# Optimization experiments

Measured on AMD Instinct MI355X. Metric: run time of the kernel, lower is better.

## Reference

```python
import jax, jax.numpy as jnp
import numpy as np

B, T, E, H = 4, 1024, 512, 8
DH = E // H  # head dim = 64


def setup_inputs() -> dict:
    key = jax.random.key(0)
    ks = jax.random.split(key, 6)
    s = 1.0 / np.sqrt(E)
    return {
        "q": jax.random.normal(ks[0], (B, T, E), dtype=jnp.float32),
        "kv": jax.random.normal(ks[1], (B, T, E), dtype=jnp.float32),
        "Wq": jax.random.normal(ks[2], (E, E), dtype=jnp.float32) * s,
        "Wk": jax.random.normal(ks[3], (E, E), dtype=jnp.float32) * s,
        "Wv": jax.random.normal(ks[4], (E, E), dtype=jnp.float32) * s,
        "Wo": jax.random.normal(ks[5], (E, E), dtype=jnp.float32) * s,
        "head_num": H,
    }


def _split_heads_dh(x, h):
    # einops 'b t (d h)' with h=head_num: head index is FASTEST in channel dim
    b, t, e = x.shape
    d = e // h
    return x.reshape(b, t, d, h).transpose(0, 3, 1, 2)  # (b, h, t, d)


def reference(q, kv, Wq, Wk, Wv, Wo, head_num):
    e = q.shape[-1]
    dk = (e // head_num) ** 0.5  # NOTE: multiplied, per original code

    qp = q @ Wq   # weights stored as (in, out); Linear(bias=False)
    kp = kv @ Wk
    vp = kv @ Wv

    query = _split_heads_dh(qp, head_num)  # (b, h, t, d)
    key = _split_heads_dh(kp, head_num)
    value = _split_heads_dh(vp, head_num)

    qf = jnp.fft.fftn(query, axes=(-2, -1))  # complex, over (t, d)
    kf = jnp.fft.fftn(key, axes=(-2, -1))

    # complex einsum, key NOT conjugated (faithful to torch source)
    energy = jnp.einsum("bhid,bhjd->bhij", qf, kf) * dk
    energy = jnp.fft.ifftn(energy, axes=(-2, -1)).real  # (b, h, t, t)

    attention = jax.nn.softmax(energy, axis=-1)
    out = jnp.einsum("bhij,bhjd->bhid", attention, value)  # (b, h, t, d)

    # einops 'b h t d -> b t (h d)': head index SLOWEST in output channel dim
    b, h, t, d = out.shape
    out = out.transpose(0, 2, 1, 3).reshape(b, t, h * d)
    return out @ Wo
```

## Files before the change

### kernel.cpp

```cpp
#include <hip/hip_runtime.h>
#include <math.h>

#define BB 4
#define TT 1024
#define EE 512
#define HH 8
#define DD 64
#define BT (BB * TT)

typedef _Float16 f16;
typedef __attribute__((ext_vector_type(8))) _Float16 f16x8;
typedef __attribute__((ext_vector_type(4))) float f32x4;

__global__ __launch_bounds__(256) void prep_w_k(const float* __restrict__ Wq,
    const float* __restrict__ Wk, const float* __restrict__ Wv,
    const float* __restrict__ Wo,
    f16* __restrict__ wqh, f16* __restrict__ wql,
    f16* __restrict__ wkh, f16* __restrict__ wkl,
    f16* __restrict__ wvh, f16* __restrict__ woh) {
    int idx = blockIdx.x * 256 + threadIdx.x;
    int k = idx & (EE - 1);
    int n = idx >> 9;
    int which = blockIdx.y;
    if (which == 0) {
        float v = Wq[k * EE + n] * 512.0f;
        f16 hi = (f16)v;
        wqh[n * EE + k] = hi;
        wql[n * EE + k] = (f16)(v - (float)hi);
    } else if (which == 1) {
        int d = n >> 3, h = n & 7;
        int sn = (((DD - d) & (DD - 1)) << 3) | h;
        float v = Wk[k * EE + sn];
        f16 hi = (f16)v;
        wkh[n * EE + k] = hi;
        wkl[n * EE + k] = (f16)(v - (float)hi);
    } else if (which == 2) {
        wvh[n * EE + k] = (f16)Wv[k * EE + n];
    } else {
        woh[n * EE + k] = (f16)Wo[k * EE + n];
    }
}

__global__ __launch_bounds__(256) void proj_k(
    const float* __restrict__ qA, const float* __restrict__ kvA,
    const f16* __restrict__ wqh, const f16* __restrict__ wql,
    const f16* __restrict__ wkh, const f16* __restrict__ wkl,
    const f16* __restrict__ wvh,
    f16* __restrict__ qhi, f16* __restrict__ qlo,
    f16* __restrict__ khi, f16* __restrict__ klo, f16* __restrict__ vT) {
    __shared__ __align__(16) f16 Ah_s[2][128][40];
    __shared__ __align__(16) f16 Al_s[2][128][40];
    __shared__ __align__(16) f16 Wh_s[2][64][40];
    __shared__ __align__(16) f16 Wl_s[2][64][40];
    __shared__ __align__(16) f16 Wv_s[2][64][40];
    f16 (*Ep)[136] = reinterpret_cast<f16(*)[136]>(&Ah_s[0][0][0]);

    const int t = threadIdx.x;
    const int w = t >> 6, l = t & 63;
    const int wm = w >> 1, wn = w & 1;
    const int fr = l & 15, fc = l >> 4;
    const int m0b = blockIdx.x * 128;
    const int n0b = blockIdx.y * 64;
    const int z   = blockIdx.z;
    const int ar = t >> 1, ak = t & 1;
    const int wr = t >> 2, wc = t & 3;

    const float* A  = z ? kvA : qA;
    const f16*   WH = z ? wkh : wqh;
    const f16*   WL = z ? wkl : wql;

    f32x4 accK[4][2], accV[4][2];
#pragma unroll
    for (int i = 0; i < 4; ++i)
#pragma unroll
        for (int j = 0; j < 2; ++j) {
            accK[i][j] = f32x4{0.f, 0.f, 0.f, 0.f};
            accV[i][j] = f32x4{0.f, 0.f, 0.f, 0.f};
        }

    float4 a4x[4];
    f16x8 wh8, wl8, wv8;

    auto loadAB = [&](int k0) {
        const float* src = A + (size_t)(m0b + ar) * EE + k0 + ak * 16;
        a4x[0] = ((const float4*)src)[0];
        a4x[1] = ((const float4*)src)[1];
        a4x[2] = ((const float4*)src)[2];
        a4x[3] = ((const float4*)src)[3];
        wh8 = *(const f16x8*)&WH[(size_t)(n0b + wr) * EE + k0 + wc * 8];
        wl8 = *(const f16x8*)&WL[(size_t)(n0b + wr) * EE + k0 + wc * 8];
        if (z) wv8 = *(const f16x8*)&wvh[(size_t)(n0b + wr) * EE + k0 + wc * 8];
    };
    auto stage = [&](int bf) {
        float xs[16] = {a4x[0].x, a4x[0].y, a4x[0].z, a4x[0].w,
                        a4x[1].x, a4x[1].y, a4x[1].z, a4x[1].w,
                        a4x[2].x, a4x[2].y, a4x[2].z, a4x[2].w,
                        a4x[3].x, a4x[3].y, a4x[3].z, a4x[3].w};
        f16x8 hi0, hi1, lo0, lo1;
#pragma unroll
        for (int e = 0; e < 8; ++e) {
            f16 ha = (f16)xs[e];     hi0[e] = ha; lo0[e] = (f16)(xs[e] - (float)ha);
            f16 hb = (f16)xs[8 + e]; hi1[e] = hb; lo1[e] = (f16)(xs[8 + e] - (float)hb);
        }
        *(f16x8*)&Ah_s[bf][ar][ak * 16]     = hi0;
        *(f16x8*)&Ah_s[bf][ar][ak * 16 + 8] = hi1;
        *(f16x8*)&Al_s[bf][ar][ak * 16]     = lo0;
        *(f16x8*)&Al_s[bf][ar][ak * 16 + 8] = lo1;
        *(f16x8*)&Wh_s[bf][wr][wc * 8] = wh8;
        *(f16x8*)&Wl_s[bf][wr][wc * 8] = wl8;
        if (z) *(f16x8*)&Wv_s[bf][wr][wc * 8] = wv8;
    };

    loadAB(0);
    stage(0);
    __syncthreads();
    int cur = 0;
    for (int ks = 0; ks < 16; ++ks) {
        if (ks < 15) loadAB((ks + 1) * 32);
        f16x8 Ahf[4], Alf[4], Bh[2], Bl[2], Bv[2];
#pragma unroll
        for (int mi = 0; mi < 4; ++mi) {
            Ahf[mi] = *(const f16x8*)&Ah_s[cur][wm * 64 + mi * 16 + fr][fc * 8];
            Alf[mi] = *(const f16x8*)&Al_s[cur][wm * 64 + mi * 16 + fr][fc * 8];
        }
#pragma unroll
        for (int nj = 0; nj < 2; ++nj) {
            Bh[nj] = *(const f16x8*)&Wh_s[cur][wn * 32 + nj * 16 + fr][fc * 8];
            Bl[nj] = *(const f16x8*)&Wl_s[cur][wn * 32 + nj * 16 + fr][fc * 8];
            if (z) Bv[nj] = *(const f16x8*)&Wv_s[cur][wn * 32 + nj * 16 + fr][fc * 8];
        }
        __builtin_amdgcn_s_setprio(1);
#pragma unroll
        for (int mi = 0; mi < 4; ++mi)
#pragma unroll
            for (int nj = 0; nj < 2; ++nj) {
                accK[mi][nj] = __builtin_amdgcn_mfma_f32_16x16x32_f16(
                    Ahf[mi], Bh[nj], accK[mi][nj], 0, 0, 0);
                accK[mi][nj] = __builtin_amdgcn_mfma_f32_16x16x32_f16(
                    Ahf[mi], Bl[nj], accK[mi][nj], 0, 0, 0);
                accK[mi][nj] = __builtin_amdgcn_mfma_f32_16x16x32_f16(
                    Alf[mi], Bh[nj], accK[mi][nj], 0, 0, 0);
                if (z)
                    accV[mi][nj] = __builtin_amdgcn_mfma_f32_16x16x32_f16(
                        Ahf[mi], Bv[nj], accV[mi][nj], 0, 0, 0);
            }
        __builtin_amdgcn_s_setprio(0);
        if (ks < 15) stage(cur ^ 1);
        __syncthreads();
        cur ^= 1;
    }

    f16* dsthi = z ? khi : qhi;
    f16* dstlo = z ? klo : qlo;
#pragma unroll
    for (int mi = 0; mi < 4; ++mi)
#pragma unroll
        for (int nj = 0; nj < 2; ++nj)
#pragma unroll
            for (int r = 0; r < 4; ++r)
                Ep[wn * 32 + nj * 16 + fr][wm * 64 + mi * 16 + fc * 4 + r] =
                    (f16)accK[mi][nj][r];
    __syncthreads();
#pragma unroll
    for (int i = 0; i < 4; ++i) {
        int task = t * 4 + i;
        int mr = task >> 3, h = task & 7;
        f16x8 v;
#pragma unroll
        for (int d = 0; d < 8; ++d) v[d] = Ep[8 * d + h][mr];
        *(f16x8*)&dsthi[((size_t)h * BT + m0b + mr) * DD + (n0b >> 3)] = v;
    }
    __syncthreads();
#pragma unroll
    for (int mi = 0; mi < 4; ++mi)
#pragma unroll
        for (int nj = 0; nj < 2; ++nj)
#pragma unroll
            for (int r = 0; r < 4; ++r) {
                float x = accK[mi][nj][r];
                f16 hh = (f16)x;
                Ep[wn * 32 + nj * 16 + fr][wm * 64 + mi * 16 + fc * 4 + r] =
                    (f16)(x - (float)hh);
            }
    __syncthreads();
#pragma unroll
    for (int i = 0; i < 4; ++i) {
        int task = t * 4 + i;
        int mr = task >> 3, h = task & 7;
        f16x8 v;
#pragma unroll
        for (int d = 0; d < 8; ++d) v[d] = Ep[8 * d + h][mr];
        *(f16x8*)&dstlo[((size_t)h * BT + m0b + mr) * DD + (n0b >> 3)] = v;
    }
    if (z) {
        __syncthreads();
#pragma unroll
        for (int mi = 0; mi < 4; ++mi)
#pragma unroll
            for (int nj = 0; nj < 2; ++nj)
#pragma unroll
                for (int r = 0; r < 4; ++r)
                    Ep[wn * 32 + nj * 16 + fr][wm * 64 + mi * 16 + fc * 4 + r] =
                        (f16)accV[mi][nj][r];
        __syncthreads();
#pragma unroll
        for (int i = 0; i < 4; ++i) {
            int task = t * 4 + i;
            int mg = task & 15, nn = task >> 4;
            int h = nn & 7, dl = nn >> 3;
            f16x8 v = *(const f16x8*)&Ep[nn][mg * 8];
            *(f16x8*)&vT[((size_t)(h * DD + (n0b >> 3) + dl)) * BT +
                         m0b + mg * 8] = v;
        }
    }
}

__global__ __launch_bounds__(256) void outmm_k(const f16* __restrict__ Af,
                                               const f16* __restrict__ WThi,
                                               float* __restrict__ out) {
    __shared__ __align__(16) f16 Ah_s[2][64][72];
    __shared__ __align__(16) f16 Wh_s[2][64][72];

    const int t = threadIdx.x;
    const int w = t >> 6, l = t & 63;
    const int wm = w >> 1, wn = w & 1;
    const int fr = l & 15, fc = l >> 4;
    const int m0b = blockIdx.x * 64;
    const int n0b = blockIdx.y * 64;
    const int sr = t >> 2, sch = t & 3;

    f32x4 acc[2][2];
#pragma unroll
    for (int i = 0; i < 2; ++i)
#pragma unroll
        for (int j = 0; j < 2; ++j) acc[i][j] = f32x4{0.f, 0.f, 0.f, 0.f};

    f16x8 af[2], wf[2];
    auto loadAB = [&](int k0) {
#pragma unroll
        for (int i = 0; i < 2; ++i) {
            af[i] = *(const f16x8*)&Af[(size_t)(m0b + sr) * EE + k0 + sch * 16 + i * 8];
            wf[i] = *(const f16x8*)&WThi[(size_t)(n0b + sr) * EE + k0 + sch * 16 + i * 8];
        }
    };
    auto stage = [&](int bf) {
#pragma unroll
        for (int i = 0; i < 2; ++i) {
            *(f16x8*)&Ah_s[bf][sr][sch * 16 + i * 8] = af[i];
            *(f16x8*)&Wh_s[bf][sr][sch * 16 + i * 8] = wf[i];
        }
    };

    loadAB(0);
    stage(0);
    __syncthreads();
    int cur = 0;
    for (int ks = 0; ks < 8; ++ks) {
        if (ks < 7) loadAB((ks + 1) * 64);
        f16x8 Ahf[2][2], Bhf[2][2];
#pragma unroll
        for (int mi = 0; mi < 2; ++mi)
#pragma unroll
            for (int kb = 0; kb < 2; ++kb)
                Ahf[mi][kb] =
                    *(const f16x8*)&Ah_s[cur][wm * 32 + mi * 16 + fr][kb * 32 + fc * 8];
#pragma unroll
        for (int nj = 0; nj < 2; ++nj)
#pragma unroll
            for (int kb = 0; kb < 2; ++kb)
                Bhf[nj][kb] =
                    *(const f16x8*)&Wh_s[cur][wn * 32 + nj * 16 + fr][kb * 32 + fc * 8];
        __builtin_amdgcn_s_setprio(1);
#pragma unroll
        for (int mi = 0; mi < 2; ++mi)
#pragma unroll
            for (int nj = 0; nj < 2; ++nj)
#pragma unroll
                for (int kb = 0; kb < 2; ++kb)
                    acc[mi][nj] = __builtin_amdgcn_mfma_f32_16x16x32_f16(
                        Ahf[mi][kb], Bhf[nj][kb], acc[mi][nj], 0, 0, 0);
        __builtin_amdgcn_s_setprio(0);
        if (ks < 7) stage(cur ^ 1);
        __syncthreads();
        cur ^= 1;
    }

    float* o = out;
#pragma unroll
    for (int mi = 0; mi < 2; ++mi)
#pragma unroll
        for (int nj = 0; nj < 2; ++nj)
#pragma unroll
            for (int r = 0; r < 4; ++r)
                o[(size_t)(m0b + wm * 32 + mi * 16 + fc * 4 + r) * EE +
                  n0b + wn * 32 + nj * 16 + fr] = acc[mi][nj][r];
}

__global__ __launch_bounds__(256) void attn_mfma_k(const f16* __restrict__ qhiP,
    const f16* __restrict__ qloP, const f16* __restrict__ khiP,
    const f16* __restrict__ kloP, const f16* __restrict__ vTP,
    f16* __restrict__ ctx) {
    __shared__ __align__(16) f16 Khi[2][64][64];
    __shared__ __align__(16) f16 Klo[2][64][64];
    __shared__ __align__(16) f16 VT[2][64][72];
    __shared__ __align__(16) f16 Pl[4][16][88];

    const int t  = threadIdx.x;
    const int w  = t >> 6;
    const int l  = t & 63;
    const int lg = l >> 4;
    const int lq = l & 15;
    const int q0 = blockIdx.x * 64 + w * 16;
    const int h  = blockIdx.y;
    const int b  = blockIdx.z;
    const size_t plane = ((size_t)h * BT + (size_t)b * TT) * DD;

    f16x8 Qhi[2], Qlo[2];
#pragma unroll
    for (int kf = 0; kf < 2; ++kf) {
        size_t qo = plane + (size_t)(q0 + lq) * DD + kf * 32 + lg * 8;
        Qhi[kf] = *(const f16x8*)&qhiP[qo];
        Qlo[kf] = *(const f16x8*)&qloP[qo];
    }

    f32x4 Oacc[4];
#pragma unroll
    for (int i = 0; i < 4; ++i) Oacc[i] = f32x4{0.f, 0.f, 0.f, 0.f};
    float m = -1e30f, lsum = 0.f;

    const int sr = t >> 2, sch = t & 3;
    f16x8 kh[2], kl[2], vv[2];

    auto loadKV = [&](int kt0) {
        size_t off = plane + (size_t)(kt0 + sr) * DD + sch * 16;
        kh[0] = *(const f16x8*)&khiP[off];
        kh[1] = *(const f16x8*)&khiP[off + 8];
        kl[0] = *(const f16x8*)&kloP[off];
        kl[1] = *(const f16x8*)&kloP[off + 8];
        size_t voff = ((size_t)h * DD + sr) * BT + (size_t)b * TT + kt0 + sch * 16;
        vv[0] = *(const f16x8*)&vTP[voff];
        vv[1] = *(const f16x8*)&vTP[voff + 8];
    };
    auto stageKV = [&](int bf) {
#pragma unroll
        for (int i = 0; i < 2; ++i) {
            int chunk = sch * 2 + i;
            int dsw = chunk ^ (sr & 7);
            *(f16x8*)&Khi[bf][sr][dsw * 8] = kh[i];
            *(f16x8*)&Klo[bf][sr][dsw * 8] = kl[i];
            *(f16x8*)&VT[bf][sr][chunk * 8] = vv[i];
        }
    };

    loadKV(0);
    stageKV(0);
    __syncthreads();
    int cur = 0;

    for (int kt0 = 0; kt0 < TT; kt0 += 64) {
        if (kt0 + 64 < TT) loadKV(kt0 + 64);

        f32x4 Sc[4];
        __builtin_amdgcn_s_setprio(1);
#pragma unroll
        for (int kt = 0; kt < 4; ++kt) {
            f32x4 c = f32x4{0.f, 0.f, 0.f, 0.f};
            int keyr = kt * 16 + lq;
#pragma unroll
            for (int kf = 0; kf < 2; ++kf) {
                int dblk = kf * 4 + lg;
                int sw = dblk ^ (keyr & 7);
                f16x8 ahi = *(const f16x8*)&Khi[cur][keyr][sw * 8];
                f16x8 alo = *(const f16x8*)&Klo[cur][keyr][sw * 8];
                c = __builtin_amdgcn_mfma_f32_16x16x32_f16(ahi, Qhi[kf], c, 0, 0, 0);
                c = __builtin_amdgcn_mfma_f32_16x16x32_f16(ahi, Qlo[kf], c, 0, 0, 0);
                c = __builtin_amdgcn_mfma_f32_16x16x32_f16(alo, Qhi[kf], c, 0, 0, 0);
            }
            Sc[kt] = c;
        }
        __builtin_amdgcn_s_setprio(0);

        float s[16];
#pragma unroll
        for (int kt = 0; kt < 4; ++kt)
#pragma unroll
            for (int r = 0; r < 4; ++r) s[kt * 4 + r] = Sc[kt][r];
        float tm = s[0];
#pragma unroll
        for (int i = 1; i < 16; ++i) tm = fmaxf(tm, s[i]);
        tm = fmaxf(tm, __shfl_xor(tm, 16));
        tm = fmaxf(tm, __shfl_xor(tm, 32));

        bool skip = __all(tm <= m + 8.0f);
        float Mn = m, corr = 1.0f;
        if (!skip) {
            Mn = fmaxf(m, tm);
            corr = __expf(m - Mn);
        }
        float ps = 0.f;
        f16 ph[16];
#pragma unroll
        for (int i = 0; i < 16; ++i) {
            float p = __expf(s[i] - Mn);
            ps += p;
            ph[i] = (f16)p;
        }
        ps += __shfl_xor(ps, 16);
        ps += __shfl_xor(ps, 32);
        if (skip) {
            lsum += ps;
        } else {
            lsum = lsum * corr + ps;
            m = Mn;
        }

#pragma unroll
        for (int kt = 0; kt < 4; ++kt)
#pragma unroll
            for (int rp = 0; rp < 4; rp += 2) {
                union { f16 h; unsigned short u; } u0, u1;
                u0.h = ph[kt * 4 + rp]; u1.h = ph[kt * 4 + rp + 1];
                unsigned int pk = ((unsigned int)u1.u << 16) | u0.u;
                *(unsigned int*)&Pl[w][lq][kt * 16 + lg * 4 + rp] = pk;
            }

        if (!skip) {
            float cq[4];
#pragma unroll
            for (int r = 0; r < 4; ++r) cq[r] = __shfl(corr, lg * 4 + r);
#pragma unroll
            for (int dvt = 0; dvt < 4; ++dvt)
#pragma unroll
                for (int r = 0; r < 4; ++r) Oacc[dvt][r] *= cq[r];
        }

        __builtin_amdgcn_s_setprio(1);
#pragma unroll
        for (int kf = 0; kf < 2; ++kf) {
            f16x8 pa = *(const f16x8*)&Pl[w][lq][kf * 32 + lg * 8];
#pragma unroll
            for (int dvt = 0; dvt < 4; ++dvt) {
                f16x8 bv = *(const f16x8*)&VT[cur][dvt * 16 + lq][kf * 32 + lg * 8];
                Oacc[dvt] = __builtin_amdgcn_mfma_f32_16x16x32_f16(pa, bv, Oacc[dvt], 0, 0, 0);
            }
        }
        __builtin_amdgcn_s_setprio(0);

        if (kt0 + 64 < TT) stageKV(cur ^ 1);
        __syncthreads();
        cur ^= 1;
    }

    float linv = 1.0f / lsum;
    float lq4[4];
#pragma unroll
    for (int r = 0; r < 4; ++r) lq4[r] = __shfl(linv, lg * 4 + r);
#pragma unroll
    for (int r = 0; r < 4; ++r) {
        f16* crow = ctx + (size_t)(b * TT + q0 + lg * 4 + r) * EE + h * DD;
#pragma unroll
        for (int dvt = 0; dvt < 4; ++dvt)
            crow[dvt * 16 + lq] = (f16)(Oacc[dvt][r] * lq4[r]);
    }
}

extern "C" void kernel_launch(void* const* d_in, const int* in_sizes, int n_in,
                              void* d_out, int out_size, void* d_ws, size_t ws_size,
                              hipStream_t stream) {
    const float* q  = (const float*)d_in[0];
    const float* kv = (const float*)d_in[1];
    const float* Wq = (const float*)d_in[2];
    const float* Wk = (const float*)d_in[3];
    const float* Wv = (const float*)d_in[4];
    const float* Wo = (const float*)d_in[5];
    float* out = (float*)d_out;

    f16* ws = (f16*)d_ws;
    const size_t PL  = (size_t)HH * BT * DD;
    const size_t WPL = (size_t)EE * EE;
    f16* qhi = ws + 0 * PL;
    f16* qlo = ws + 1 * PL;
    f16* khi = ws + 2 * PL;
    f16* klo = ws + 3 * PL;
    f16* vT  = ws + 4 * PL;
    f16* ctx = ws + 5 * PL;
    f16* wqh = ws + 6 * PL;
    f16* wql = wqh + 1 * WPL;
    f16* wkh = wqh + 2 * WPL;
    f16* wkl = wqh + 3 * WPL;
    f16* wvh = wqh + 4 * WPL;
    f16* woh = wqh + 5 * WPL;

    prep_w_k<<<dim3((EE * EE) / 256, 4), dim3(256), 0, stream>>>(
        Wq, Wk, Wv, Wo, wqh, wql, wkh, wkl, wvh, woh);

    proj_k<<<dim3(BT / 128, EE / 64, 2), dim3(256), 0, stream>>>(
        q, kv, wqh, wql, wkh, wkl, wvh, qhi, qlo, khi, klo, vT);

    attn_mfma_k<<<dim3(TT / 64, HH, BB), dim3(256), 0, stream>>>(
        qhi, qlo, khi, klo, vT, ctx);

    outmm_k<<<dim3(BT / 64, EE / 64), dim3(256), 0, stream>>>(ctx, woh, out);
}
```

Measured before the change: 78.31 us.

## Pre-split activations into fp16 hi/lo, load V directly, swizzle attention block order

The fp32-to-fp16 hi/lo split of q and kv moves out of the projection GEMM and into the prep kernel, so the split runs once per element instead of once per column tile and the GEMM loads half the bytes per A element. The attention kernel stops staging V through LDS and instead loads V fragments from global memory into registers each tile, which frees LDS. It also launches a 1D grid with a swizzled block-to-(batch, head, query-tile) mapping aimed at L2 locality. The cost is an extra pass writing and reading four activation-sized fp16 buffers, plus V global loads issued inside the loop with less latency hiding.

```diff
diff --git a/kernel.cpp b/kernel.cpp
--- a/kernel.cpp
+++ b/kernel.cpp
@@ -12,37 +12,61 @@
 typedef __attribute__((ext_vector_type(8))) _Float16 f16x8;
 typedef __attribute__((ext_vector_type(4))) float f32x4;
 
-__global__ __launch_bounds__(256) void prep_w_k(const float* __restrict__ Wq,
-    const float* __restrict__ Wk, const float* __restrict__ Wv,
-    const float* __restrict__ Wo,
+__global__ __launch_bounds__(256) void prep_k(
+    const float* __restrict__ q, const float* __restrict__ kv,
+    const float* __restrict__ Wq, const float* __restrict__ Wk,
+    const float* __restrict__ Wv, const float* __restrict__ Wo,
     f16* __restrict__ wqh, f16* __restrict__ wql,
     f16* __restrict__ wkh, f16* __restrict__ wkl,
-    f16* __restrict__ wvh, f16* __restrict__ woh) {
-    int idx = blockIdx.x * 256 + threadIdx.x;
-    int k = idx & (EE - 1);
-    int n = idx >> 9;
-    int which = blockIdx.y;
-    if (which == 0) {
-        float v = Wq[k * EE + n] * 512.0f;
-        f16 hi = (f16)v;
-        wqh[n * EE + k] = hi;
-        wql[n * EE + k] = (f16)(v - (float)hi);
-    } else if (which == 1) {
-        int d = n >> 3, h = n & 7;
-        int sn = (((DD - d) & (DD - 1)) << 3) | h;
-        float v = Wk[k * EE + sn];
-        f16 hi = (f16)v;
-        wkh[n * EE + k] = hi;
-        wkl[n * EE + k] = (f16)(v - (float)hi);
-    } else if (which == 2) {
-        wvh[n * EE + k] = (f16)Wv[k * EE + n];
+    f16* __restrict__ wvh, f16* __restrict__ woh,
+    f16* __restrict__ qAhi, f16* __restrict__ qAlo,
+    f16* __restrict__ kvAhi, f16* __restrict__ kvAlo) {
+    const int t = threadIdx.x;
+    const int y = blockIdx.y;
+    if (y < 4) {
+        int idx = blockIdx.x * 256 + t;
+        int k = idx & (EE - 1);
+        int n = idx >> 9;
+        if (y == 0) {
+            float v = Wq[k * EE + n] * 512.0f;
+            f16 hi = (f16)v;
+            wqh[n * EE + k] = hi;
+            wql[n * EE + k] = (f16)(v - (float)hi);
+        } else if (y == 1) {
+            int d = n >> 3, h = n & 7;
+            int sn = (((DD - d) & (DD - 1)) << 3) | h;
+            float v = Wk[k * EE + sn];
+            f16 hi = (f16)v;
+            wkh[n * EE + k] = hi;
+            wkl[n * EE + k] = (f16)(v - (float)hi);
+        } else if (y == 2) {
+            wvh[n * EE + k] = (f16)Wv[k * EE + n];
+        } else {
+            woh[n * EE + k] = (f16)Wo[k * EE + n];
+        }
     } else {
-        woh[n * EE + k] = (f16)Wo[k * EE + n];
+        const float* src = (y == 4) ? q : kv;
+        f16* dh = (y == 4) ? qAhi : kvAhi;
+        f16* dl = (y == 4) ? qAlo : kvAlo;
+        int base = (blockIdx.x * 256 + t) * 8;
+        float4 a = *(const float4*)&src[base];
+        float4 c = *(const float4*)&src[base + 4];
+        float xs[8] = {a.x, a.y, a.z, a.w, c.x, c.y, c.z, c.w};
+        f16x8 hi, lo;
+#pragma unroll
+        for (int e = 0; e < 8; ++e) {
+            f16 hh = (f16)xs[e];
+            hi[e] = hh;
+            lo[e] = (f16)(xs[e] - (float)hh);
+        }
+        *(f16x8*)&dh[base] = hi;
+        *(f16x8*)&dl[base] = lo;
     }
 }
 
 __global__ __launch_bounds__(256) void proj_k(
-    const float* __restrict__ qA, const float* __restrict__ kvA,
+    const f16* __restrict__ qAhi, const f16* __restrict__ qAlo,
+    const f16* __restrict__ kvAhi, const f16* __restrict__ kvAlo,
     const f16* __restrict__ wqh, const f16* __restrict__ wql,
     const f16* __restrict__ wkh, const f16* __restrict__ wkl,
     const f16* __restrict__ wvh,
@@ -65,9 +89,10 @@
     const int ar = t >> 1, ak = t & 1;
     const int wr = t >> 2, wc = t & 3;
 
-    const float* A  = z ? kvA : qA;
-    const f16*   WH = z ? wkh : wqh;
-    const f16*   WL = z ? wkl : wql;
+    const f16* AH = z ? kvAhi : qAhi;
+    const f16* AL = z ? kvAlo : qAlo;
+    const f16* WH = z ? wkh : wqh;
+    const f16* WL = z ? wkl : wql;
 
     f32x4 accK[4][2], accV[4][2];
 #pragma unroll
@@ -78,34 +103,24 @@
             accV[i][j] = f32x4{0.f, 0.f, 0.f, 0.f};
         }
 
-    float4 a4x[4];
-    f16x8 wh8, wl8, wv8;
+    f16x8 ah8[2], al8[2], wh8, wl8, wv8;
 
     auto loadAB = [&](int k0) {
-        const float* src = A + (size_t)(m0b + ar) * EE + k0 + ak * 16;
-        a4x[0] = ((const float4*)src)[0];
-        a4x[1] = ((const float4*)src)[1];
-        a4x[2] = ((const float4*)src)[2];
-        a4x[3] = ((const float4*)src)[3];
-        wh8 = *(const f16x8*)&WH[(size_t)(n0b + wr) * EE + k0 + wc * 8];
-        wl8 = *(const f16x8*)&WL[(size_t)(n0b + wr) * EE + k0 + wc * 8];
-        if (z) wv8 = *(const f16x8*)&wvh[(size_t)(n0b + wr) * EE + k0 + wc * 8];
+        size_t aoff = (size_t)(m0b + ar) * EE + k0 + ak * 16;
+        ah8[0] = *(const f16x8*)&AH[aoff];
+        ah8[1] = *(const f16x8*)&AH[aoff + 8];
+        al8[0] = *(const f16x8*)&AL[aoff];
+        al8[1] = *(const f16x8*)&AL[aoff + 8];
+        size_t woff = (size_t)(n0b + wr) * EE + k0 + wc * 8;
+        wh8 = *(const f16x8*)&WH[woff];
+        wl8 = *(const f16x8*)&WL[woff];
+        if (z) wv8 = *(const f16x8*)&wvh[woff];
     };
     auto stage = [&](int bf) {
-        float xs[16] = {a4x[0].x, a4x[0].y, a4x[0].z, a4x[0].w,
-                        a4x[1].x, a4x[1].y, a4x[1].z, a4x[1].w,
-                        a4x[2].x, a4x[2].y, a4x[2].z, a4x[2].w,
-                        a4x[3].x, a4x[3].y, a4x[3].z, a4x[3].w};
-        f16x8 hi0, hi1, lo0, lo1;
-#pragma unroll
-        for (int e = 0; e < 8; ++e) {
-            f16 ha = (f16)xs[e];     hi0[e] = ha; lo0[e] = (f16)(xs[e] - (float)ha);
-            f16 hb = (f16)xs[8 + e]; hi1[e] = hb; lo1[e] = (f16)(xs[8 + e] - (float)hb);
-        }
-        *(f16x8*)&Ah_s[bf][ar][ak * 16]     = hi0;
-        *(f16x8*)&Ah_s[bf][ar][ak * 16 + 8] = hi1;
-        *(f16x8*)&Al_s[bf][ar][ak * 16]     = lo0;
-        *(f16x8*)&Al_s[bf][ar][ak * 16 + 8] = lo1;
+        *(f16x8*)&Ah_s[bf][ar][ak * 16]     = ah8[0];
+        *(f16x8*)&Ah_s[bf][ar][ak * 16 + 8] = ah8[1];
+        *(f16x8*)&Al_s[bf][ar][ak * 16]     = al8[0];
+        *(f16x8*)&Al_s[bf][ar][ak * 16 + 8] = al8[1];
         *(f16x8*)&Wh_s[bf][wr][wc * 8] = wh8;
         *(f16x8*)&Wl_s[bf][wr][wc * 8] = wl8;
         if (z) *(f16x8*)&Wv_s[bf][wr][wc * 8] = wv8;
@@ -285,15 +300,14 @@
         cur ^= 1;
     }
 
-    float* o = out;
 #pragma unroll
     for (int mi = 0; mi < 2; ++mi)
 #pragma unroll
         for (int nj = 0; nj < 2; ++nj)
 #pragma unroll
             for (int r = 0; r < 4; ++r)
-                o[(size_t)(m0b + wm * 32 + mi * 16 + fc * 4 + r) * EE +
-                  n0b + wn * 32 + nj * 16 + fr] = acc[mi][nj][r];
+                out[(size_t)(m0b + wm * 32 + mi * 16 + fc * 4 + r) * EE +
+                    n0b + wn * 32 + nj * 16 + fr] = acc[mi][nj][r];
 }
 
 __global__ __launch_bounds__(256) void attn_mfma_k(const f16* __restrict__ qhiP,
@@ -302,17 +316,20 @@
     f16* __restrict__ ctx) {
     __shared__ __align__(16) f16 Khi[2][64][64];
     __shared__ __align__(16) f16 Klo[2][64][64];
-    __shared__ __align__(16) f16 VT[2][64][72];
     __shared__ __align__(16) f16 Pl[4][16][88];
+
+    const int bid = blockIdx.x;
+    const int swz = (bid & 7) * 64 + (bid >> 3);
+    const int bx = swz & 15;
+    const int h  = (swz >> 4) & 7;
+    const int b  = swz >> 7;
 
     const int t  = threadIdx.x;
     const int w  = t >> 6;
     const int l  = t & 63;
     const int lg = l >> 4;
     const int lq = l & 15;
-    const int q0 = blockIdx.x * 64 + w * 16;
-    const int h  = blockIdx.y;
-    const int b  = blockIdx.z;
+    const int q0 = bx * 64 + w * 16;
     const size_t plane = ((size_t)h * BT + (size_t)b * TT) * DD;
 
     f16x8 Qhi[2], Qlo[2];
@@ -322,6 +339,7 @@
         Qhi[kf] = *(const f16x8*)&qhiP[qo];
         Qlo[kf] = *(const f16x8*)&qloP[qo];
     }
+    const f16* vbase = vTP + ((size_t)h * DD + lq) * BT + (size_t)b * TT + lg * 8;
 
     f32x4 Oacc[4];
 #pragma unroll
@@ -329,36 +347,39 @@
     float m = -1e30f, lsum = 0.f;
 
     const int sr = t >> 2, sch = t & 3;
-    f16x8 kh[2], kl[2], vv[2];
-
-    auto loadKV = [&](int kt0) {
+    f16x8 kh[2], kl[2];
+
+    auto loadK = [&](int kt0) {
         size_t off = plane + (size_t)(kt0 + sr) * DD + sch * 16;
         kh[0] = *(const f16x8*)&khiP[off];
         kh[1] = *(const f16x8*)&khiP[off + 8];
         kl[0] = *(const f16x8*)&kloP[off];
         kl[1] = *(const f16x8*)&kloP[off + 8];
-        size_t voff = ((size_t)h * DD + sr) * BT + (size_t)b * TT + kt0 + sch * 16;
-        vv[0] = *(const f16x8*)&vTP[voff];
-        vv[1] = *(const f16x8*)&vTP[voff + 8];
     };
-    auto stageKV = [&](int bf) {
+    auto stageK = [&](int bf) {
 #pragma unroll
         for (int i = 0; i < 2; ++i) {
             int chunk = sch * 2 + i;
             int dsw = chunk ^ (sr & 7);
             *(f16x8*)&Khi[bf][sr][dsw * 8] = kh[i];
             *(f16x8*)&Klo[bf][sr][dsw * 8] = kl[i];
-            *(f16x8*)&VT[bf][sr][chunk * 8] = vv[i];
         }
     };
 
-    loadKV(0);
-    stageKV(0);
+    loadK(0);
+    stageK(0);
     __syncthreads();
     int cur = 0;
 
     for (int kt0 = 0; kt0 < TT; kt0 += 64) {
-        if (kt0 + 64 < TT) loadKV(kt0 + 64);
+        f16x8 bv[2][4];
+#pragma unroll
+        for (int kf = 0; kf < 2; ++kf)
+#pragma unroll
+            for (int dvt = 0; dvt < 4; ++dvt)
+                bv[kf][dvt] = *(const f16x8*)&vbase[(size_t)dvt * 16 * BT +
+                                                    kt0 + kf * 32];
+        if (kt0 + 64 < TT) loadK(kt0 + 64);
 
         f32x4 Sc[4];
         __builtin_amdgcn_s_setprio(1);
@@ -439,14 +460,13 @@
         for (int kf = 0; kf < 2; ++kf) {
             f16x8 pa = *(const f16x8*)&Pl[w][lq][kf * 32 + lg * 8];
 #pragma unroll
-            for (int dvt = 0; dvt < 4; ++dvt) {
-                f16x8 bv = *(const f16x8*)&VT[cur][dvt * 16 + lq][kf * 32 + lg * 8];
-                Oacc[dvt] = __builtin_amdgcn_mfma_f32_16x16x32_f16(pa, bv, Oacc[dvt], 0, 0, 0);
-            }
+            for (int dvt = 0; dvt < 4; ++dvt)
+                Oacc[dvt] = __builtin_amdgcn_mfma_f32_16x16x32_f16(
+                    pa, bv[kf][dvt], Oacc[dvt], 0, 0, 0);
         }
         __builtin_amdgcn_s_setprio(0);
 
-        if (kt0 + 64 < TT) stageKV(cur ^ 1);
+        if (kt0 + 64 < TT) stageK(cur ^ 1);
         __syncthreads();
         cur ^= 1;
     }
@@ -478,26 +498,32 @@
     f16* ws = (f16*)d_ws;
     const size_t PL  = (size_t)HH * BT * DD;
     const size_t WPL = (size_t)EE * EE;
-    f16* qhi = ws + 0 * PL;
-    f16* qlo = ws + 1 * PL;
-    f16* khi = ws + 2 * PL;
-    f16* klo = ws + 3 * PL;
-    f16* vT  = ws + 4 * PL;
-    f16* ctx = ws + 5 * PL;
-    f16* wqh = ws + 6 * PL;
+    f16* qhi   = ws + 0 * PL;
+    f16* qlo   = ws + 1 * PL;
+    f16* khi   = ws + 2 * PL;
+    f16* klo   = ws + 3 * PL;
+    f16* vT    = ws + 4 * PL;
+    f16* ctx   = ws + 5 * PL;
+    f16* qAhi  = ws + 6 * PL;
+    f16* qAlo  = ws + 7 * PL;
+    f16* kvAhi = ws + 8 * PL;
+    f16* kvAlo = ws + 9 * PL;
+    f16* wqh = ws + 10 * PL;
     f16* wql = wqh + 1 * WPL;
     f16* wkh = wqh + 2 * WPL;
     f16* wkl = wqh + 3 * WPL;
     f16* wvh = wqh + 4 * WPL;
     f16* woh = wqh + 5 * WPL;
 
-    prep_w_k<<<dim3((EE * EE) / 256, 4), dim3(256), 0, stream>>>(
-        Wq, Wk, Wv, Wo, wqh, wql, wkh, wkl, wvh, woh);
+    prep_k<<<dim3(1024, 6), dim3(256), 0, stream>>>(
+        q, kv, Wq, Wk, Wv, Wo, wqh, wql, wkh, wkl, wvh, woh,
+        qAhi, qAlo, kvAhi, kvAlo);
 
     proj_k<<<dim3(BT / 128, EE / 64, 2), dim3(256), 0, stream>>>(
-        q, kv, wqh, wql, wkh, wkl, wvh, qhi, qlo, khi, klo, vT);
-
-    attn_mfma_k<<<dim3(TT / 64, HH, BB), dim3(256), 0, stream>>>(
+        qAhi, qAlo, kvAhi, kvAlo, wqh, wql, wkh, wkl, wvh,
+        qhi, qlo, khi, klo, vT);
+
+    attn_mfma_k<<<dim3(512), dim3(256), 0, stream>>>(
         qhi, qlo, khi, klo, vT, ctx);
 
     outmm_k<<<dim3(BT / 64, EE / 64), dim3(256), 0, stream>>>(ctx, woh, out);
```

Measured after the change: 82.98 us. 1.06x slower.
